# Kernel optimization log

Measured on AMD Instinct MI355X. Metric: run time of the kernel, lower is better.

## Reference

```python
import jax, jax.numpy as jnp
import numpy as np

B, L, C = 32, 2048, 32
PL, STRIDE = 16, 16
P = L // PL
D, H_ENC, H_DEC, K, NH = 64, 256, 256, 512, 4
BETA, EPS, Q_EPS, CW = 0.25, 1e-5, 1e-5, 0.2


def setup_inputs() -> dict:
    key = jax.random.key(0)
    ks = jax.random.split(key, 16)
    g = lambda k, sh: 0.02 * jax.random.normal(k, sh, dtype=jnp.float32)
    return {
        'x': jax.random.normal(ks[0], (B, L, C), dtype=jnp.float32),
        'revin_w': jnp.ones((C,), jnp.float32), 'revin_b': jnp.zeros((C,), jnp.float32),
        'inp_W': g(ks[1], (PL, D)), 'inp_b': jnp.zeros((D,), jnp.float32),
        'Wq': g(ks[2], (D, D)), 'bq': jnp.zeros((D,), jnp.float32),
        'Wk': g(ks[3], (D, D)), 'bk': jnp.zeros((D,), jnp.float32),
        'Wv': g(ks[4], (D, D)), 'bv': jnp.zeros((D,), jnp.float32),
        'Wo': g(ks[5], (D, D)), 'bo': jnp.zeros((D,), jnp.float32),
        'ln1_g': jnp.ones((D,), jnp.float32), 'ln1_b': jnp.zeros((D,), jnp.float32),
        'ffn_W1': g(ks[6], (D, H_ENC)), 'ffn_b1': jnp.zeros((H_ENC,), jnp.float32),
        'ffn_W2': g(ks[7], (H_ENC, D)), 'ffn_b2': jnp.zeros((D,), jnp.float32),
        'ln2_g': jnp.ones((D,), jnp.float32), 'ln2_b': jnp.zeros((D,), jnp.float32),
        'codebook': jax.random.uniform(ks[8], (K, D), jnp.float32, -1.0 / K, 1.0 / K),
        'dec_W1': g(ks[9], (D, H_DEC)), 'dec_b1': jnp.zeros((H_DEC,), jnp.float32),
        'dec_W2': g(ks[10], (H_DEC, PL)), 'dec_b2': jnp.zeros((PL,), jnp.float32),
        'dec_Wr': g(ks[11], (D, PL)), 'dec_br': jnp.zeros((PL,), jnp.float32),
        'dec_ln_g': jnp.ones((PL,), jnp.float32), 'dec_ln_b': jnp.zeros((PL,), jnp.float32),
    }


def _layernorm(x, g, b):
    m = jnp.mean(x, -1, keepdims=True)
    v = jnp.mean((x - m) ** 2, -1, keepdims=True)
    return (x - m) * jax.lax.rsqrt(v + EPS) * g + b


def reference(x, revin_w, revin_b, inp_W, inp_b, Wq, bq, Wk, bk, Wv, bv, Wo, bo,
              ln1_g, ln1_b, ffn_W1, ffn_b1, ffn_W2, ffn_b2, ln2_g, ln2_b, codebook,
              dec_W1, dec_b1, dec_W2, dec_b2, dec_Wr, dec_br, dec_ln_g, dec_ln_b):
    # --- RevIN norm (stats over time dim) ---
    mean = jnp.mean(x, axis=1, keepdims=True)              # [B,1,C]
    std = jnp.sqrt(jnp.var(x, axis=1, keepdims=True) + EPS)
    xn = (x - mean) / std * revin_w + revin_b
    # --- patchify: [B,C,L] -> [B*C, P, PL] ---
    patches = jnp.transpose(xn, (0, 2, 1)).reshape(B * C, P, PL)
    # --- MHEncoder ---
    h = patches @ inp_W + inp_b                            # [N,P,D]
    dh = D // NH
    q = (h @ Wq + bq).reshape(-1, P, NH, dh)
    k = (h @ Wk + bk).reshape(-1, P, NH, dh)
    v = (h @ Wv + bv).reshape(-1, P, NH, dh)
    scores = jnp.einsum('nqhd,nkhd->nhqk', q, k) / np.sqrt(dh).astype(np.float32)
    attn = jax.nn.softmax(scores, axis=-1)
    a = jnp.einsum('nhqk,nkhd->nqhd', attn, v).reshape(-1, P, D)
    a = a @ Wo + bo
    h = _layernorm(h + a, ln1_g, ln1_b)
    ff = jax.nn.relu(h @ ffn_W1 + ffn_b1) @ ffn_W2 + ffn_b2
    h = _layernorm(h + ff, ln2_g, ln2_b)
    z = h.reshape(B, C, P, D)
    # --- ClusterQuantizer ---
    z2 = jnp.sum(z * z, -1, keepdims=True)                 # [B,V,P,1]
    e2 = jnp.sum(codebook * codebook, -1)                  # [K]
    ze = jnp.einsum('bvpd,kd->bvpk', z, codebook)
    dist = z2 + e2 - 2.0 * ze                              # [B,V,P,K]
    indices = jnp.argmin(dist, axis=-1)                    # [B,V,P] int
    z_q = codebook[indices]
    z_q_st = z + jax.lax.stop_gradient(z_q - z)
    codebook_loss = jnp.mean((z_q - jax.lax.stop_gradient(z)) ** 2)
    commitment_loss = jnp.mean((z - jax.lax.stop_gradient(z_q)) ** 2)
    cluster_loss = codebook_loss + BETA * commitment_loss
    counts = jnp.zeros((K,), jnp.float32).at[indices.ravel()].add(1.0)
    probs = counts / (counts.sum() + EPS)
    perplexity = jnp.exp(-jnp.sum(probs * jnp.log(probs + EPS)))
    # --- FFN decoder ---
    y = jax.nn.relu(z_q_st @ dec_W1 + dec_b1) @ dec_W2 + dec_b2
    y = y + z_q_st @ dec_Wr + dec_br
    recon_patches = _layernorm(y, dec_ln_g, dec_ln_b)      # [B,V,P,PL]
    recon = jnp.transpose(recon_patches.reshape(B, C, L), (0, 2, 1))  # [B,L,C]
    # --- RevIN denorm ---
    r = (recon - revin_b) / (revin_w + EPS * EPS) * std + mean
    rec_loss = jnp.mean((x - r) ** 2)
    loss_total = rec_loss + CW * cluster_loss
    return (loss_total, rec_loss, z_q_st, r, indices, perplexity)
```

## Files before the change

### kernel.cpp

```cpp
#include <hip/hip_runtime.h>
#include <math.h>

#define TPB 256

#define B_  32
#define L_  2048
#define C_  32
#define PL_ 16
#define P_  128
#define D_  64
#define HE_ 256
#define HD_ 256
#define K_  512
#define N_  1024
#define M_  131072

#define EPS_  1e-5f
#define BETA_ 0.25f
#define CW_   0.2f

#define OUT_LOSS 0
#define OUT_REC  1
#define OUT_ZQ   2
#define OUT_R    8388610
#define OUT_IDX  10485762
#define OUT_PERP 10616834

#define WS_MEAN   0
#define WS_STD    1024
#define WS_QT     2048
#define WS_KT     6144
#define WS_VT     10240
#define WS_E2     34816
#define WS_COUNTS 35328
#define WS_CPART  35840
#define WS_H0     36864
#define WS_H1     8425472
#define WS_RPART  WS_H1

__global__ void k_prep(const float* __restrict__ Wq, const float* __restrict__ Wk,
                       const float* __restrict__ Wv,
                       const float* __restrict__ cb, float* __restrict__ ws) {
    int g = blockIdx.x * TPB + threadIdx.x;
    if (g < 4096) { int t = g >> 6, j = g & 63; ws[WS_QT + g] = Wq[j * D_ + t]; }
    else if (g < 8192) { int g2 = g - 4096; int t = g2 >> 6, j = g2 & 63; ws[WS_KT + g2] = Wk[j * D_ + t]; }
    else if (g < 12288) { int g2 = g - 8192; int t = g2 >> 6, j = g2 & 63; ws[WS_VT + g2] = Wv[j * D_ + t]; }
    if (g < K_) {
        float s = 0.f;
        for (int j = 0; j < D_; j++) { float v = cb[g * D_ + j]; s += v * v; }
        ws[WS_E2 + g] = s;
    }
}

__global__ void k_stats(const float* __restrict__ x, float* __restrict__ ws) {
    int bc = blockIdx.x;
    int b = bc >> 5, c = bc & 31;
    const float* xp = x + (size_t)b * L_ * C_ + c;
    float s = 0.f, s2 = 0.f;
    for (int l = threadIdx.x; l < L_; l += TPB) { float v = xp[(size_t)l * C_]; s += v; s2 += v * v; }
    __shared__ float sh[TPB], sh2[TPB];
    sh[threadIdx.x] = s; sh2[threadIdx.x] = s2; __syncthreads();
    for (int o2 = 128; o2 > 0; o2 >>= 1) {
        if (threadIdx.x < o2) { sh[threadIdx.x] += sh[threadIdx.x + o2]; sh2[threadIdx.x] += sh2[threadIdx.x + o2]; }
        __syncthreads();
    }
    if (threadIdx.x == 0) {
        float m = sh[0] / (float)L_;
        float var = sh2[0] / (float)L_ - m * m;
        ws[WS_MEAN + bc] = m;
        ws[WS_STD + bc] = sqrtf(var + EPS_);
    }
}

__global__ __launch_bounds__(TPB) void k_embed(
    const float* __restrict__ x, const float* __restrict__ rw, const float* __restrict__ rb,
    const float* __restrict__ inpW, const float* __restrict__ inpb, float* __restrict__ ws) {
    int idx = blockIdx.x * TPB + threadIdx.x;
    int row = idx >> 6, d = idx & 63;
    int n = row >> 7, p = row & 127;
    int b = n >> 5, c = n & 31;
    float m = ws[WS_MEAN + n], sd = ws[WS_STD + n];
    float w = rw[c], bb = rb[c];
    const float* xp = x + (size_t)b * L_ * C_ + (size_t)p * PL_ * C_ + c;
    float acc = inpb[d];
#pragma unroll
    for (int j = 0; j < PL_; j++) {
        float xv = xp[(size_t)j * C_];
        float xn = (xv - m) / sd * w + bb;
        acc += xn * inpW[j * D_ + d];
    }
    ws[WS_H0 + (size_t)idx] = acc;
}

#define HSS  68
#define HS_  0
#define KH_  8704
#define VH_  10752
#define SMF  12800

__global__ __launch_bounds__(TPB) void k_attn(
    float* __restrict__ ws,
    const float* __restrict__ bq, const float* __restrict__ bk, const float* __restrict__ bv) {
    __shared__ float sm[SMF];
    const int tid = threadIdx.x;
    const int n = blockIdx.x >> 2, hh = blockIdx.x & 3;
    const float* h0 = ws + WS_H0 + (size_t)n * (P_ * D_);
    float* agl = ws + WS_H1 + (size_t)n * (P_ * D_);

    {
        const float4* h04 = (const float4*)h0;
#pragma unroll
        for (int it = 0; it < 8; ++it) {
            int e = tid + it * 256;
            int r = e >> 4, j4 = e & 15;
            *(float4*)(sm + HS_ + r * HSS + j4 * 4) = h04[e];
        }
    }
    __syncthreads();

    const int t_ = tid & 15, ib = tid >> 4;
    const float4* WqT4 = (const float4*)(ws + WS_QT);
    const float4* WkT4 = (const float4*)(ws + WS_KT);
    const float4* WvT4 = (const float4*)(ws + WS_VT);

    {
        float4 wk[16], wv[16];
        const float4* kr = WkT4 + (size_t)(hh * 16 + t_) * 16;
        const float4* vr = WvT4 + (size_t)(hh * 16 + t_) * 16;
#pragma unroll
        for (int j4 = 0; j4 < 16; j4++) { wk[j4] = kr[j4]; wv[j4] = vr[j4]; }
        float bbk = bk[hh * 16 + t_], bbv = bv[hh * 16 + t_];
#pragma unroll
        for (int it = 0; it < 8; it++) {
            int i2 = ib + it * 16;
            const float4* hr = (const float4*)(sm + HS_ + i2 * HSS);
            float accK = bbk, accV = bbv;
#pragma unroll
            for (int j4 = 0; j4 < 16; j4++) {
                float4 h4 = hr[j4];
                float4 k4 = wk[j4], v4 = wv[j4];
                accK += h4.x * k4.x + h4.y * k4.y + h4.z * k4.z + h4.w * k4.w;
                accV += h4.x * v4.x + h4.y * v4.y + h4.z * v4.z + h4.w * v4.w;
            }
            sm[KH_ + i2 * 16 + t_] = accK;
            sm[VH_ + i2 * 16 + t_] = accV;
        }
    }
    const int i = tid >> 1, half = tid & 1;
    float q0[8], q1[8];
    {
        float4 hreg[16];
        const float4* hr = (const float4*)(sm + HS_ + i * HSS);
#pragma unroll
        for (int j4 = 0; j4 < 16; j4++) hreg[j4] = hr[j4];
        float qh[8];
#pragma unroll
        for (int u = 0; u < 8; u++) {
            const float4* wr = WqT4 + (size_t)(hh * 16 + half * 8 + u) * 16;
            float acc = bq[hh * 16 + half * 8 + u];
#pragma unroll
            for (int j4 = 0; j4 < 16; j4++) {
                float4 w4 = wr[j4];
                acc += hreg[j4].x * w4.x + hreg[j4].y * w4.y + hreg[j4].z * w4.z + hreg[j4].w * w4.w;
            }
            qh[u] = acc;
        }
#pragma unroll
        for (int u = 0; u < 8; u++) {
            float oth = __shfl_xor(qh[u], 1);
            q0[u] = half ? oth : qh[u];
            q1[u] = half ? qh[u] : oth;
        }
    }
    __syncthreads();
    float S = 0.f;
    float o[16];
#pragma unroll
    for (int u = 0; u < 16; u++) o[u] = 0.f;
    const float4* kh4 = (const float4*)(sm + KH_);
    const float4* vh4 = (const float4*)(sm + VH_);
#pragma unroll 4
    for (int m2 = 0; m2 < 64; m2++) {
        int m = m2 * 2 + half;
        float4 a0 = kh4[m * 4 + 0], a1 = kh4[m * 4 + 1], a2 = kh4[m * 4 + 2], a3 = kh4[m * 4 + 3];
        float sp = q0[0] * a0.x + q0[1] * a0.y + q0[2] * a0.z + q0[3] * a0.w
                 + q0[4] * a1.x + q0[5] * a1.y + q0[6] * a1.z + q0[7] * a1.w
                 + q1[0] * a2.x + q1[1] * a2.y + q1[2] * a2.z + q1[3] * a2.w
                 + q1[4] * a3.x + q1[5] * a3.y + q1[6] * a3.z + q1[7] * a3.w;
        float p = __expf(sp * 0.25f);
        S += p;
        float4 v0 = vh4[m * 4 + 0], v1 = vh4[m * 4 + 1], v2 = vh4[m * 4 + 2], v3 = vh4[m * 4 + 3];
        o[0] += p * v0.x; o[1] += p * v0.y; o[2] += p * v0.z; o[3] += p * v0.w;
        o[4] += p * v1.x; o[5] += p * v1.y; o[6] += p * v1.z; o[7] += p * v1.w;
        o[8] += p * v2.x; o[9] += p * v2.y; o[10] += p * v2.z; o[11] += p * v2.w;
        o[12] += p * v3.x; o[13] += p * v3.y; o[14] += p * v3.z; o[15] += p * v3.w;
    }
    {
        S += __shfl_xor(S, 1);
        float inv = 1.f / S;
        float wv[8];
#pragma unroll
        for (int u = 0; u < 8; u++) {
            float lo = o[u] + __shfl_xor(o[u], 1);
            float hi = o[8 + u] + __shfl_xor(o[8 + u], 1);
            wv[u] = (half ? hi : lo) * inv;
        }
        float4 r0, r1;
        r0.x = wv[0]; r0.y = wv[1]; r0.z = wv[2]; r0.w = wv[3];
        r1.x = wv[4]; r1.y = wv[5]; r1.z = wv[6]; r1.w = wv[7];
        float4* ap4 = (float4*)(agl + (size_t)i * D_ + hh * 16 + half * 8);
        ap4[0] = r0; ap4[1] = r1;
    }
}

#define FHS  68

__global__ __launch_bounds__(TPB) void k_woffn(
    float* __restrict__ ws, const float* __restrict__ Wo, const float* __restrict__ bo,
    const float* __restrict__ g1, const float* __restrict__ b1,
    const float* __restrict__ fW1, const float* __restrict__ fb1,
    const float* __restrict__ fW2, const float* __restrict__ fb2,
    const float* __restrict__ g2, const float* __restrict__ b2) {
    __shared__ float bufA[64][FHS];
    __shared__ float hT[64][FHS];
    const int tid = threadIdx.x;
    const int row0 = blockIdx.x * 64;
    const float* aog = ws + WS_H1 + (size_t)row0 * D_;

    {
        const float4* ao4 = (const float4*)aog;
#pragma unroll
        for (int it = 0; it < 4; ++it) {
            int e = tid + it * 256;
            int r = e >> 4, j4 = e & 15;
            float4 v = ao4[e];
            bufA[j4 * 4 + 0][r] = v.x; bufA[j4 * 4 + 1][r] = v.y;
            bufA[j4 * 4 + 2][r] = v.z; bufA[j4 * 4 + 3][r] = v.w;
        }
    }
    const int ty = tid >> 4, tx = tid & 15;
    float acc[4][4];
    {
        float4 bb = ((const float4*)bo)[tx];
#pragma unroll
        for (int r = 0; r < 4; r++) { acc[r][0] = bb.x; acc[r][1] = bb.y; acc[r][2] = bb.z; acc[r][3] = bb.w; }
    }
    __syncthreads();
    const float4* Wo4 = (const float4*)Wo;
#pragma unroll 4
    for (int j = 0; j < 64; ++j) {
        float4 a = *(const float4*)&bufA[j][ty * 4];
        float4 w = Wo4[j * 16 + tx];
        float ar[4] = {a.x, a.y, a.z, a.w}, wr[4] = {w.x, w.y, w.z, w.w};
#pragma unroll
        for (int r = 0; r < 4; r++)
#pragma unroll
            for (int c = 0; c < 4; c++) acc[r][c] += ar[r] * wr[c];
    }
    float h1v[4][4];
    {
        const float4* h04 = (const float4*)(ws + WS_H0 + (size_t)row0 * D_);
        float4 gg = ((const float4*)g1)[tx], bbn = ((const float4*)b1)[tx];
#pragma unroll
        for (int r = 0; r < 4; r++) {
            float4 res = h04[(ty * 4 + r) * 16 + tx];
            acc[r][0] += res.x; acc[r][1] += res.y; acc[r][2] += res.z; acc[r][3] += res.w;
            float s = acc[r][0] + acc[r][1] + acc[r][2] + acc[r][3];
            s += __shfl_xor(s, 1); s += __shfl_xor(s, 2); s += __shfl_xor(s, 4); s += __shfl_xor(s, 8);
            float mean_ = s * (1.f / 64.f);
            float vv = 0.f;
#pragma unroll
            for (int c = 0; c < 4; c++) { float d_ = acc[r][c] - mean_; vv += d_ * d_; }
            vv += __shfl_xor(vv, 1); vv += __shfl_xor(vv, 2); vv += __shfl_xor(vv, 4); vv += __shfl_xor(vv, 8);
            float rstd = 1.f / sqrtf(vv * (1.f / 64.f) + EPS_);
            h1v[r][0] = (acc[r][0] - mean_) * rstd * gg.x + bbn.x;
            h1v[r][1] = (acc[r][1] - mean_) * rstd * gg.y + bbn.y;
            h1v[r][2] = (acc[r][2] - mean_) * rstd * gg.z + bbn.z;
            h1v[r][3] = (acc[r][3] - mean_) * rstd * gg.w + bbn.w;
        }
    }
#pragma unroll
    for (int r = 0; r < 4; r++)
#pragma unroll
        for (int c = 0; c < 4; c++) hT[tx * 4 + c][ty * 4 + r] = h1v[r][c];
    const float4* W14 = (const float4*)fW1;
    const float4* W24 = (const float4*)fW2;
    float outv[4][4];
    {
        float4 bb = ((const float4*)fb2)[tx];
#pragma unroll
        for (int r = 0; r < 4; r++) { outv[r][0] = bb.x; outv[r][1] = bb.y; outv[r][2] = bb.z; outv[r][3] = bb.w; }
    }
    __syncthreads();

    for (int tc = 0; tc < 4; ++tc) {
        float a2[4][4];
        {
            float4 bb1 = ((const float4*)fb1)[tc * 16 + tx];
#pragma unroll
            for (int r = 0; r < 4; r++) { a2[r][0] = bb1.x; a2[r][1] = bb1.y; a2[r][2] = bb1.z; a2[r][3] = bb1.w; }
        }
#pragma unroll 4
        for (int j = 0; j < 64; ++j) {
            float4 a = *(const float4*)&hT[j][ty * 4];
            float4 w = W14[j * 64 + tc * 16 + tx];
            float ar[4] = {a.x, a.y, a.z, a.w}, wr[4] = {w.x, w.y, w.z, w.w};
#pragma unroll
            for (int r = 0; r < 4; r++)
#pragma unroll
                for (int c = 0; c < 4; c++) a2[r][c] += ar[r] * wr[c];
        }
        __syncthreads();
#pragma unroll
        for (int r = 0; r < 4; r++)
#pragma unroll
            for (int c = 0; c < 4; c++) bufA[tx * 4 + c][ty * 4 + r] = fmaxf(a2[r][c], 0.f);
        __syncthreads();
#pragma unroll 4
        for (int h = 0; h < 64; ++h) {
            float4 a = *(const float4*)&bufA[h][ty * 4];
            float4 w = W24[(tc * 64 + h) * 16 + tx];
            float ar[4] = {a.x, a.y, a.z, a.w}, wr[4] = {w.x, w.y, w.z, w.w};
#pragma unroll
            for (int r = 0; r < 4; r++)
#pragma unroll
                for (int c = 0; c < 4; c++) outv[r][c] += ar[r] * wr[c];
        }
    }
    {
        float4 gg = ((const float4*)g2)[tx], bb = ((const float4*)b2)[tx];
        float4* zp = (float4*)(ws + WS_H0 + (size_t)row0 * D_);
#pragma unroll
        for (int r = 0; r < 4; r++) {
            outv[r][0] += h1v[r][0]; outv[r][1] += h1v[r][1];
            outv[r][2] += h1v[r][2]; outv[r][3] += h1v[r][3];
            float s = outv[r][0] + outv[r][1] + outv[r][2] + outv[r][3];
            s += __shfl_xor(s, 1); s += __shfl_xor(s, 2); s += __shfl_xor(s, 4); s += __shfl_xor(s, 8);
            float mean_ = s * (1.f / 64.f);
            float vv = 0.f;
#pragma unroll
            for (int c = 0; c < 4; c++) { float d_ = outv[r][c] - mean_; vv += d_ * d_; }
            vv += __shfl_xor(vv, 1); vv += __shfl_xor(vv, 2); vv += __shfl_xor(vv, 4); vv += __shfl_xor(vv, 8);
            float rstd = 1.f / sqrtf(vv * (1.f / 64.f) + EPS_);
            float4 z;
            z.x = (outv[r][0] - mean_) * rstd * gg.x + bb.x;
            z.y = (outv[r][1] - mean_) * rstd * gg.y + bb.y;
            z.z = (outv[r][2] - mean_) * rstd * gg.z + bb.z;
            z.w = (outv[r][3] - mean_) * rstd * gg.w + bb.w;
            zp[(ty * 4 + r) * 16 + tx] = z;
        }
    }
}

#define QROWS 128
#define QKT   64
#define ZTS   132
#define CBS   68

__global__ __launch_bounds__(TPB) void k_quant(
    float* __restrict__ ws, const float* __restrict__ cb, float* __restrict__ out) {
    __shared__ float zT[64][ZTS];
    __shared__ float cbT[64][CBS];
    __shared__ float z2s[QROWS];
    __shared__ float e2t[QKT];
    __shared__ int   ridx[QROWS];
    __shared__ float red[TPB];

    const int tid = threadIdx.x;
    const int row0 = blockIdx.x * QROWS;
    const float* zg = ws + WS_H0 + (size_t)row0 * D_;
    const float4* zg4 = (const float4*)zg;
    const float4* cbg4 = (const float4*)cb;

    {
        int j4 = tid >> 4;
#pragma unroll
        for (int it = 0; it < 8; ++it) {
            int r = (tid & 15) + it * 16;
            float4 v = zg4[r * 16 + j4];
            zT[j4 * 4 + 0][r] = v.x; zT[j4 * 4 + 1][r] = v.y;
            zT[j4 * 4 + 2][r] = v.z; zT[j4 * 4 + 3][r] = v.w;
        }
    }
    if (tid < QROWS) {
        const float4* zr = (const float4*)(zg + (size_t)tid * D_);
        float s = 0.f;
#pragma unroll
        for (int j = 0; j < 16; j++) { float4 v = zr[j]; s += v.x * v.x + v.y * v.y + v.z * v.z + v.w * v.w; }
        z2s[tid] = s;
    }

    const int ty = tid >> 4, tx = tid & 15;
    float best[8]; int bidx[8];
#pragma unroll
    for (int u = 0; u < 8; u++) { best[u] = 3.4e38f; bidx[u] = 0; }

    for (int t = 0; t < K_ / QKT; ++t) {
        const int k0 = t * QKT;
        __syncthreads();
        {
            int j4 = tid >> 4;
#pragma unroll
            for (int it = 0; it < 4; ++it) {
                int kk = (tid & 15) + it * 16;
                float4 v = cbg4[(size_t)(k0 + kk) * 16 + j4];
                cbT[j4 * 4 + 0][kk] = v.x; cbT[j4 * 4 + 1][kk] = v.y;
                cbT[j4 * 4 + 2][kk] = v.z; cbT[j4 * 4 + 3][kk] = v.w;
            }
        }
        if (tid < QKT) e2t[tid] = ws[WS_E2 + k0 + tid];
        __syncthreads();

        float acc[8][4];
#pragma unroll
        for (int u = 0; u < 8; u++)
#pragma unroll
            for (int c = 0; c < 4; c++) acc[u][c] = 0.f;

        for (int j = 0; j < 64; ++j) {
            float4 a0 = *(const float4*)&zT[j][ty * 8];
            float4 a1 = *(const float4*)&zT[j][ty * 8 + 4];
            float4 b0 = *(const float4*)&cbT[j][tx * 4];
            float ar[8] = {a0.x, a0.y, a0.z, a0.w, a1.x, a1.y, a1.z, a1.w};
            float br[4] = {b0.x, b0.y, b0.z, b0.w};
#pragma unroll
            for (int u = 0; u < 8; u++)
#pragma unroll
                for (int c = 0; c < 4; c++) acc[u][c] += ar[u] * br[c];
        }

#pragma unroll
        for (int u = 0; u < 8; u++) {
            float z2v = z2s[ty * 8 + u];
#pragma unroll
            for (int c = 0; c < 4; c++) {
                float dist = (z2v + e2t[tx * 4 + c]) - 2.f * acc[u][c];
                int kidx = k0 + tx * 4 + c;
                if (dist < best[u]) { best[u] = dist; bidx[u] = kidx; }
            }
        }
    }

#pragma unroll
    for (int m = 1; m <= 8; m <<= 1) {
#pragma unroll
        for (int u = 0; u < 8; u++) {
            float ob = __shfl_xor(best[u], m, 64);
            int oi = __shfl_xor(bidx[u], m, 64);
            if (ob < best[u] || (ob == best[u] && oi < bidx[u])) { best[u] = ob; bidx[u] = oi; }
        }
    }
    if (tx == 0) {
#pragma unroll
        for (int u = 0; u < 8; u++) ridx[ty * 8 + u] = bidx[u];
    }
    __syncthreads();

    if (tid < QROWS) {
        int bi = ridx[tid];
        out[OUT_IDX + row0 + tid] = (float)bi;
        atomicAdd((unsigned int*)ws + WS_COUNTS + bi, 1u);
    }
    {
        int r = tid >> 1, half = tid & 1;
        int bi = ridx[r];
        const float4* cw = (const float4*)(cb + (size_t)bi * D_ + half * 32);
        const float4* zr4 = (const float4*)(zg + (size_t)r * D_ + half * 32);
        float2* zqo = (float2*)(out + OUT_ZQ + (size_t)(row0 + r) * D_ + half * 32);
        float csum = 0.f;
#pragma unroll
        for (int j4 = 0; j4 < 8; ++j4) {
            float4 w = cw[j4]; float4 zz = zr4[j4];
            float d0 = w.x - zz.x, d1 = w.y - zz.y, d2 = w.z - zz.z, d3 = w.w - zz.w;
            csum += d0 * d0 + d1 * d1 + d2 * d2 + d3 * d3;
            float2 p0; p0.x = w.x; p0.y = w.y; zqo[j4 * 2] = p0;
            float2 p1; p1.x = w.z; p1.y = w.w; zqo[j4 * 2 + 1] = p1;
        }
        red[tid] = csum;
    }
    __syncthreads();
    for (int o2 = 128; o2 > 0; o2 >>= 1) {
        if (tid < o2) red[tid] += red[tid + o2];
        __syncthreads();
    }
    if (tid == 0) ws[WS_CPART + blockIdx.x] = red[0];
}

#define DR_ 64

__global__ __launch_bounds__(TPB) void k_dec(
    float* __restrict__ ws, const float* __restrict__ x, const float* __restrict__ cb,
    const float* __restrict__ dW1, const float* __restrict__ db1,
    const float* __restrict__ dW2, const float* __restrict__ db2,
    const float* __restrict__ dWr, const float* __restrict__ dbr,
    const float* __restrict__ lng, const float* __restrict__ lnb,
    const float* __restrict__ rw, const float* __restrict__ rb,
    float* __restrict__ out) {
    __shared__ float zqT[64][FHS];
    __shared__ float Hc[64][FHS];
    __shared__ int   ridx[DR_];
    __shared__ float red[TPB];
    const int tid = threadIdx.x;
    const int row0 = blockIdx.x * DR_;
    if (tid < DR_) ridx[tid] = (int)out[OUT_IDX + row0 + tid];
    __syncthreads();
    {
        const float4* cb4 = (const float4*)cb;
#pragma unroll
        for (int it = 0; it < 4; ++it) {
            int e = tid + it * 256;
            int r = e >> 4, j4 = e & 15;
            float4 v = cb4[(size_t)ridx[r] * 16 + j4];
            zqT[j4 * 4 + 0][r] = v.x; zqT[j4 * 4 + 1][r] = v.y;
            zqT[j4 * 4 + 2][r] = v.z; zqT[j4 * 4 + 3][r] = v.w;
        }
    }
    const int ty = tid >> 4, tx = tid & 15;
    const float4* dW14 = (const float4*)dW1;
    float out4[4];
    {
        float b0 = db2[tx] + dbr[tx];
#pragma unroll
        for (int r = 0; r < 4; r++) out4[r] = b0;
    }
    __syncthreads();

    for (int tc = 0; tc < 4; ++tc) {
        float acc[4][4];
        {
            float4 bb1 = ((const float4*)db1)[tc * 16 + tx];
#pragma unroll
            for (int r = 0; r < 4; r++) { acc[r][0] = bb1.x; acc[r][1] = bb1.y; acc[r][2] = bb1.z; acc[r][3] = bb1.w; }
        }
#pragma unroll 4
        for (int j = 0; j < 64; ++j) {
            float4 a = *(const float4*)&zqT[j][ty * 4];
            float4 w = dW14[j * 64 + tc * 16 + tx];
            float ar[4] = {a.x, a.y, a.z, a.w}, wr[4] = {w.x, w.y, w.z, w.w};
#pragma unroll
            for (int r = 0; r < 4; r++)
#pragma unroll
                for (int c = 0; c < 4; c++) acc[r][c] += ar[r] * wr[c];
        }
        __syncthreads();
#pragma unroll
        for (int r = 0; r < 4; r++)
#pragma unroll
            for (int c = 0; c < 4; c++) Hc[tx * 4 + c][ty * 4 + r] = fmaxf(acc[r][c], 0.f);
        __syncthreads();
#pragma unroll 8
        for (int h = 0; h < 64; ++h) {
            float4 a = *(const float4*)&Hc[h][ty * 4];
            float w = dW2[(tc * 64 + h) * 16 + tx];
            out4[0] += a.x * w; out4[1] += a.y * w; out4[2] += a.z * w; out4[3] += a.w * w;
        }
    }
#pragma unroll 8
    for (int j = 0; j < 64; ++j) {
        float4 a = *(const float4*)&zqT[j][ty * 4];
        float w = dWr[j * 16 + tx];
        out4[0] += a.x * w; out4[1] += a.y * w; out4[2] += a.z * w; out4[3] += a.w * w;
    }
    const int n = row0 >> 7;
    const int b = n >> 5, c = n & 31;
    const float sd = ws[WS_STD + n], mn = ws[WS_MEAN + n];
    const float inv = 1.f / (rw[c] + EPS_ * EPS_);
    const float rbc = rb[c];
    const float lg = lng[tx], lb = lnb[tx];
    float part = 0.f;
#pragma unroll
    for (int r = 0; r < 4; r++) {
        float v = out4[r];
        float s = v;
        s += __shfl_xor(s, 1); s += __shfl_xor(s, 2); s += __shfl_xor(s, 4); s += __shfl_xor(s, 8);
        float mean_ = s * (1.f / 16.f);
        float d_ = v - mean_;
        float vv = d_ * d_;
        vv += __shfl_xor(vv, 1); vv += __shfl_xor(vv, 2); vv += __shfl_xor(vv, 4); vv += __shfl_xor(vv, 8);
        float rstd = 1.f / sqrtf(vv * (1.f / 16.f) + EPS_);
        float yv = d_ * rstd * lg + lb;
        float rr = (yv - rbc) * inv * sd + mn;
        int row = row0 + ty * 4 + r;
        int p = row & 127;
        size_t xi = (size_t)b * L_ * C_ + (size_t)(p * PL_ + tx) * C_ + c;
        out[OUT_R + xi] = rr;
        float dx = x[xi] - rr; part += dx * dx;
    }
    red[tid] = part;
    __syncthreads();
    for (int o2 = 128; o2 > 0; o2 >>= 1) {
        if (tid < o2) red[tid] += red[tid + o2];
        __syncthreads();
    }
    if (tid == 0) ws[WS_RPART + blockIdx.x] = red[0];
}

__global__ void k_final(float* __restrict__ ws, float* __restrict__ out) {
    __shared__ float sh[TPB];
    int tid = threadIdx.x;
    float cs = 0.f;
    for (int i2 = tid; i2 < 1024; i2 += TPB) cs += ws[WS_CPART + i2];
    sh[tid] = cs; __syncthreads();
    for (int o2 = 128; o2 > 0; o2 >>= 1) { if (tid < o2) sh[tid] += sh[tid + o2]; __syncthreads(); }
    float csum = sh[0]; __syncthreads();
    float rs = 0.f;
    for (int i2 = tid; i2 < 2048; i2 += TPB) rs += ws[WS_RPART + i2];
    sh[tid] = rs; __syncthreads();
    for (int o2 = 128; o2 > 0; o2 >>= 1) { if (tid < o2) sh[tid] += sh[tid + o2]; __syncthreads(); }
    float rsum = sh[0]; __syncthreads();
    const unsigned int* counts = (const unsigned int*)ws + WS_COUNTS;
    float H = 0.f;
    for (int k2 = tid; k2 < K_; k2 += TPB) {
        float p = (float)counts[k2] / (131072.f + EPS_);
        H += p * logf(p + EPS_);
    }
    sh[tid] = H; __syncthreads();
    for (int o2 = 128; o2 > 0; o2 >>= 1) { if (tid < o2) sh[tid] += sh[tid + o2]; __syncthreads(); }
    if (tid == 0) {
        float rec = rsum / 2097152.f;
        float msd = csum / 8388608.f;
        float cl = (1.f + BETA_) * msd;
        out[OUT_LOSS] = rec + CW_ * cl;
        out[OUT_REC] = rec;
        out[OUT_PERP] = expf(-sh[0]);
    }
}

extern "C" void kernel_launch(void* const* d_in, const int* in_sizes, int n_in,
                              void* d_out, int out_size, void* d_ws, size_t ws_size,
                              hipStream_t stream) {
    const float* x    = (const float*)d_in[0];
    const float* rw   = (const float*)d_in[1];
    const float* rb   = (const float*)d_in[2];
    const float* inpW = (const float*)d_in[3];
    const float* inpb = (const float*)d_in[4];
    const float* Wq   = (const float*)d_in[5];
    const float* bq   = (const float*)d_in[6];
    const float* Wk   = (const float*)d_in[7];
    const float* bk   = (const float*)d_in[8];
    const float* Wv   = (const float*)d_in[9];
    const float* bv   = (const float*)d_in[10];
    const float* Wo   = (const float*)d_in[11];
    const float* bo   = (const float*)d_in[12];
    const float* g1   = (const float*)d_in[13];
    const float* b1   = (const float*)d_in[14];
    const float* fW1  = (const float*)d_in[15];
    const float* fb1  = (const float*)d_in[16];
    const float* fW2  = (const float*)d_in[17];
    const float* fb2  = (const float*)d_in[18];
    const float* g2   = (const float*)d_in[19];
    const float* b2   = (const float*)d_in[20];
    const float* cb   = (const float*)d_in[21];
    const float* dW1  = (const float*)d_in[22];
    const float* db1  = (const float*)d_in[23];
    const float* dW2  = (const float*)d_in[24];
    const float* db2  = (const float*)d_in[25];
    const float* dWr  = (const float*)d_in[26];
    const float* dbr  = (const float*)d_in[27];
    const float* lng  = (const float*)d_in[28];
    const float* lnb  = (const float*)d_in[29];
    float* ws  = (float*)d_ws;
    float* out = (float*)d_out;

    hipMemsetAsync((char*)d_ws + (size_t)WS_COUNTS * 4, 0, 512 * 4, stream);
    k_prep<<<48, TPB, 0, stream>>>(Wq, Wk, Wv, cb, ws);
    k_stats<<<N_, TPB, 0, stream>>>(x, ws);
    k_embed<<<(M_ * D_) / TPB, TPB, 0, stream>>>(x, rw, rb, inpW, inpb, ws);
    k_attn<<<N_ * 4, TPB, 0, stream>>>(ws, bq, bk, bv);
    k_woffn<<<M_ / 64, TPB, 0, stream>>>(ws, Wo, bo, g1, b1, fW1, fb1, fW2, fb2, g2, b2);
    k_quant<<<M_ / QROWS, TPB, 0, stream>>>(ws, cb, out);
    k_dec<<<M_ / DR_, TPB, 0, stream>>>(ws, x, cb, dW1, db1, dW2, db2, dWr, dbr, lng, lnb, rw, rb, out);
    k_final<<<1, TPB, 0, stream>>>(ws, out);
}
```

Before: 712.3 us.

## Vectorize stats and embed kernels, remap attention blocks for XCD locality

k_stats now handles four channels per block with float4 loads, using 256 blocks instead of 1024, so strided scalar reads become wider coalesced reads. k_embed gives each thread four output features via float4 weight loads and a float4 store, which cuts redundant x reads by a factor of four. k_attn remaps blockIdx so the four head-blocks of a series land on the same XCD, aiming for better L2 reuse of h0. The cost is fewer blocks in k_stats, which lowers parallelism, and the remap assumes round-robin XCD dispatch.

```diff
diff --git a/kernel.cpp b/kernel.cpp
--- a/kernel.cpp
+++ b/kernel.cpp
@@ -53,43 +53,59 @@
 }
 
 __global__ void k_stats(const float* __restrict__ x, float* __restrict__ ws) {
-    int bc = blockIdx.x;
-    int b = bc >> 5, c = bc & 31;
-    const float* xp = x + (size_t)b * L_ * C_ + c;
-    float s = 0.f, s2 = 0.f;
-    for (int l = threadIdx.x; l < L_; l += TPB) { float v = xp[(size_t)l * C_]; s += v; s2 += v * v; }
-    __shared__ float sh[TPB], sh2[TPB];
+    const int blk = blockIdx.x;
+    const int b = blk >> 3, c0 = (blk & 7) * 4;
+    const float4* xp = (const float4*)(x + (size_t)b * L_ * C_ + c0);
+    float4 s = {0.f, 0.f, 0.f, 0.f}, s2 = {0.f, 0.f, 0.f, 0.f};
+    for (int l = threadIdx.x; l < L_; l += TPB) {
+        float4 v = xp[(size_t)l * 8];
+        s.x += v.x; s.y += v.y; s.z += v.z; s.w += v.w;
+        s2.x += v.x * v.x; s2.y += v.y * v.y; s2.z += v.z * v.z; s2.w += v.w * v.w;
+    }
+    __shared__ float4 sh[TPB], sh2[TPB];
     sh[threadIdx.x] = s; sh2[threadIdx.x] = s2; __syncthreads();
     for (int o2 = 128; o2 > 0; o2 >>= 1) {
-        if (threadIdx.x < o2) { sh[threadIdx.x] += sh[threadIdx.x + o2]; sh2[threadIdx.x] += sh2[threadIdx.x + o2]; }
+        if (threadIdx.x < o2) {
+            float4 a = sh[threadIdx.x], bq_ = sh[threadIdx.x + o2];
+            a.x += bq_.x; a.y += bq_.y; a.z += bq_.z; a.w += bq_.w; sh[threadIdx.x] = a;
+            float4 a2 = sh2[threadIdx.x], b2_ = sh2[threadIdx.x + o2];
+            a2.x += b2_.x; a2.y += b2_.y; a2.z += b2_.z; a2.w += b2_.w; sh2[threadIdx.x] = a2;
+        }
         __syncthreads();
     }
     if (threadIdx.x == 0) {
-        float m = sh[0] / (float)L_;
-        float var = sh2[0] / (float)L_ - m * m;
-        ws[WS_MEAN + bc] = m;
-        ws[WS_STD + bc] = sqrtf(var + EPS_);
+        float sv[4] = {sh[0].x, sh[0].y, sh[0].z, sh[0].w};
+        float qv[4] = {sh2[0].x, sh2[0].y, sh2[0].z, sh2[0].w};
+#pragma unroll
+        for (int u = 0; u < 4; u++) {
+            float m = sv[u] / (float)L_;
+            float var = qv[u] / (float)L_ - m * m;
+            ws[WS_MEAN + b * 32 + c0 + u] = m;
+            ws[WS_STD + b * 32 + c0 + u] = sqrtf(var + EPS_);
+        }
     }
 }
 
 __global__ __launch_bounds__(TPB) void k_embed(
     const float* __restrict__ x, const float* __restrict__ rw, const float* __restrict__ rb,
     const float* __restrict__ inpW, const float* __restrict__ inpb, float* __restrict__ ws) {
-    int idx = blockIdx.x * TPB + threadIdx.x;
-    int row = idx >> 6, d = idx & 63;
+    int g = blockIdx.x * TPB + threadIdx.x;
+    int row = g >> 4, d4 = g & 15;
     int n = row >> 7, p = row & 127;
     int b = n >> 5, c = n & 31;
     float m = ws[WS_MEAN + n], sd = ws[WS_STD + n];
     float w = rw[c], bb = rb[c];
     const float* xp = x + (size_t)b * L_ * C_ + (size_t)p * PL_ * C_ + c;
-    float acc = inpb[d];
+    const float4* W4 = (const float4*)inpW;
+    float4 acc = ((const float4*)inpb)[d4];
 #pragma unroll
     for (int j = 0; j < PL_; j++) {
         float xv = xp[(size_t)j * C_];
         float xn = (xv - m) / sd * w + bb;
-        acc += xn * inpW[j * D_ + d];
-    }
-    ws[WS_H0 + (size_t)idx] = acc;
+        float4 wv = W4[j * 16 + d4];
+        acc.x += xn * wv.x; acc.y += xn * wv.y; acc.z += xn * wv.z; acc.w += xn * wv.w;
+    }
+    ((float4*)(ws + WS_H0))[g] = acc;
 }
 
 #define HSS  68
@@ -103,7 +119,8 @@
     const float* __restrict__ bq, const float* __restrict__ bk, const float* __restrict__ bv) {
     __shared__ float sm[SMF];
     const int tid = threadIdx.x;
-    const int n = blockIdx.x >> 2, hh = blockIdx.x & 3;
+    const int xcd = blockIdx.x & 7, iw = blockIdx.x >> 3;
+    const int n = xcd * 128 + (iw >> 2), hh = iw & 3;
     const float* h0 = ws + WS_H0 + (size_t)n * (P_ * D_);
     float* agl = ws + WS_H1 + (size_t)n * (P_ * D_);
 
@@ -664,8 +681,8 @@
 
     hipMemsetAsync((char*)d_ws + (size_t)WS_COUNTS * 4, 0, 512 * 4, stream);
     k_prep<<<48, TPB, 0, stream>>>(Wq, Wk, Wv, cb, ws);
-    k_stats<<<N_, TPB, 0, stream>>>(x, ws);
-    k_embed<<<(M_ * D_) / TPB, TPB, 0, stream>>>(x, rw, rb, inpW, inpb, ws);
+    k_stats<<<256, TPB, 0, stream>>>(x, ws);
+    k_embed<<<(M_ * 16) / TPB, TPB, 0, stream>>>(x, rw, rb, inpW, inpb, ws);
     k_attn<<<N_ * 4, TPB, 0, stream>>>(ws, bq, bk, bv);
     k_woffn<<<M_ / 64, TPB, 0, stream>>>(ws, Wo, bo, g1, b1, fW1, fb1, fW2, fb2, g2, b2);
     k_quant<<<M_ / QROWS, TPB, 0, stream>>>(ws, cb, out);
```

Measured after the change: 670.1 us. 5.9% less time.
